# Performance work log

Hardware: AMD Instinct MI355X
Metric: run time of the kernel (lower is better)

Reference implementation:

```python
import jax, jax.numpy as jnp
import numpy as np
import math

IN_DIM = 3
N_LEVELS = 16
N_FEATS = 2
LOG2_HASHMAP = 19
BASE_RES = 16
DESIRED_RES = 2048
N_POINTS = 1048576
# first in_dim hash primes from the torch module; all fit in uint32
PRIMES = np.array([1, 2654435761, 805459861], dtype=np.uint32)


def _level_params():
    # faithful to the torch code: growth exponent divides by (base_resolution - 1)
    beta = math.exp((math.log(DESIRED_RES) - math.log(BASE_RES)) / (BASE_RES - 1))
    res = [math.floor(BASE_RES * beta ** i) for i in range(N_LEVELS)]
    hms = [min(r ** IN_DIM, 2 ** LOG2_HASHMAP) for r in res]
    return res, hms


def setup_inputs() -> dict:
    key = jax.random.key(0)
    kx, kt = jax.random.split(key)
    x = jax.random.uniform(kx, (N_POINTS, IN_DIM), dtype=jnp.float32)
    # kaiming_uniform(a=sqrt(5)) on [hashmap, n_feats] -> bound = sqrt(1/2)
    bound = math.sqrt(0.5)
    tables = jax.random.uniform(kt, (N_LEVELS, 2 ** LOG2_HASHMAP, N_FEATS),
                                dtype=jnp.float32, minval=-bound, maxval=bound)
    return {"x": x, "tables": tables}


def _forward(x, tables):
    res, hms = _level_params()
    neighbors = np.arange(1 << IN_DIM, dtype=np.int64).reshape(-1, 1)   # [8,1]
    dims = np.arange(IN_DIM, dtype=np.int64).reshape(1, -1)             # [1,3]
    bin_mask = jnp.asarray((neighbors & (1 << dims)) == 0)              # [8,3] bool
    primes = jnp.asarray(PRIMES)                                        # [3] uint32
    outs = [x]  # include_input=True
    for l in range(N_LEVELS):
        xs = x * jnp.float32(res[l])                    # [N,3]
        xi = jnp.floor(xs).astype(jnp.int32)            # torch .long() trunc; x>=0 so floor==trunc
        xf = xs - xi.astype(xs.dtype)                   # fractional part (no grad via xi)
        xi = xi[..., None, :]                           # [N,1,3]
        xf = xf[..., None, :]                           # [N,1,3]
        idx = jnp.where(bin_mask, xi, xi + 1).astype(jnp.uint32)         # [N,8,3]
        w = jnp.prod(jnp.where(bin_mask, 1.0 - xf, xf), axis=-1, keepdims=True)  # [N,8,1]
        # hash: (idx * prime) mod 2^32 (uint32 wraparound == int64 mul & 0xFFFFFFFF), xor-fold, mod size
        h = idx * primes                                # [N,8,3] uint32
        h = h[..., 0] ^ h[..., 1] ^ h[..., 2]           # [N,8]
        h = (h % jnp.uint32(hms[l])).astype(jnp.int32)
        emb = tables[l][h]                              # [N,8,F] gather
        outs.append(jnp.sum(emb * w, axis=-2))          # [N,F]
    return jnp.concatenate(outs, axis=-1)               # [N, 3 + 16*2]


def reference(x, tables):
    return _forward(x, tables)
```

## Files before the change

kernel.cpp:

```cpp
#include <hip/hip_runtime.h>
#include <math.h>
#include <stdint.h>

#define NPTS   1048576
#define NLEV   16
#define TPB    256
#define PPT    8
#define CHUNK  (TPB * PPT)
#define ROW    35
#define TBL_ENTRIES (1u << 19)

typedef float f4 __attribute__((ext_vector_type(4)));
typedef float f2 __attribute__((ext_vector_type(2)));

struct LevelParams {
    float    resf;
    uint32_t hm;
    uint32_t is_pow2;
    uint32_t use_nt;
    uint64_t magic;
};
struct LPAll { LevelParams lv[NLEV]; };

__device__ __forceinline__ void hash_gather_point(
    float xv0, float xv1, float xv2,
    const LevelParams& P, const f2* __restrict__ tbl,
    float& acc0, float& acc1)
{
    const float xs0 = xv0 * P.resf, xs1 = xv1 * P.resf, xs2 = xv2 * P.resf;
    const float f0 = floorf(xs0), f1 = floorf(xs1), f2v = floorf(xs2);
    const float t0 = xs0 - f0, t1 = xs1 - f1, t2 = xs2 - f2v;

    const unsigned a0 = (unsigned)(int)f0;
    const unsigned a1 = a0 + 1u;
    const unsigned b0 = (unsigned)(int)f1 * 2654435761u;
    const unsigned b1 = ((unsigned)(int)f1 + 1u) * 2654435761u;
    const unsigned c0 = (unsigned)(int)f2v * 805459861u;
    const unsigned c1 = ((unsigned)(int)f2v + 1u) * 805459861u;

    const float wa0 = 1.f - t0, wa1 = t0;
    const float wb0 = 1.f - t1, wb1 = t1;
    const float wc0 = 1.f - t2, wc1 = t2;

    const uint32_t hmv  = P.hm;
    const uint32_t mask = hmv - 1u;
    const uint64_t M    = P.magic;
    const bool     p2   = (P.is_pow2 != 0);
    const bool     nt   = (P.use_nt != 0);

    unsigned hi[8];
    #pragma unroll
    for (int n = 0; n < 8; ++n) {
        unsigned h = ((n & 1) ? a1 : a0)
                   ^ ((n & 2) ? b1 : b0)
                   ^ ((n & 4) ? c1 : c0);
        if (p2) {
            hi[n] = h & mask;
        } else {
            uint64_t low = M * (uint64_t)h;
            hi[n] = (uint32_t)(((__uint128_t)low * hmv) >> 64);
        }
    }
    f2 e[8];
    #pragma unroll
    for (int n = 0; n < 8; ++n)
        e[n] = nt ? __builtin_nontemporal_load(&tbl[hi[n]]) : tbl[hi[n]];

    acc0 = 0.f; acc1 = 0.f;
    #pragma unroll
    for (int n = 0; n < 8; ++n) {
        float w = (((n & 1) ? wa1 : wa0) * ((n & 2) ? wb1 : wb0))
                  * ((n & 4) ? wc1 : wc0);
        acc0 = fmaf(e[n].x, w, acc0);
        acc1 = fmaf(e[n].y, w, acc1);
    }
}

__global__ __launch_bounds__(TPB)
void hashgrid_gather(const float* __restrict__ x,
                     const float* __restrict__ tables,
                     float* __restrict__ ws,
                     LPAll lp, int base)
{
    const int tid = threadIdx.x;
    const int lvl = base + (blockIdx.x & 7);
    const int p0  = (blockIdx.x >> 3) * CHUNK;

    const LevelParams P   = lp.lv[lvl];
    const f2*         tbl = (const f2*)(tables + (size_t)lvl * TBL_ENTRIES * 2);
    const float*      xp  = x + (size_t)p0 * 3;
    f2* wrow = (f2*)ws + (size_t)lvl * NPTS + p0;

    #pragma unroll
    for (int k = 0; k < PPT; ++k) {
        const int pi = tid + k * TPB;
        const float xv0 = __builtin_nontemporal_load(&xp[pi * 3 + 0]);
        const float xv1 = __builtin_nontemporal_load(&xp[pi * 3 + 1]);
        const float xv2 = __builtin_nontemporal_load(&xp[pi * 3 + 2]);
        float acc0, acc1;
        hash_gather_point(xv0, xv1, xv2, P, tbl, acc0, acc1);
        f2 v; v.x = acc0; v.y = acc1;
        __builtin_nontemporal_store(v, &wrow[pi]);
    }
}

__global__ __launch_bounds__(TPB)
void hashgrid_interleave(const float* __restrict__ x,
                         const float* __restrict__ ws,
                         float* __restrict__ out)
{
    __shared__ float srow[TPB * ROW];
    const int tid = threadIdx.x;
    const int p0  = blockIdx.x * TPB;

    const float* xblk = x + (size_t)p0 * 3;
    #pragma unroll
    for (int j = 0; j < 3; ++j) {
        int idx = tid + j * TPB;
        int p = idx / 3, c = idx - p * 3;
        srow[p * ROW + c] = __builtin_nontemporal_load(&xblk[idx]);
    }
    const f2* wsv = (const f2*)ws;
    #pragma unroll
    for (int l = 0; l < NLEV; ++l) {
        f2 v = __builtin_nontemporal_load(&wsv[(size_t)l * NPTS + p0 + tid]);
        srow[tid * ROW + 3 + 2 * l] = v.x;
        srow[tid * ROW + 4 + 2 * l] = v.y;
    }
    __syncthreads();

    f4*       outv = (f4*)(out + (size_t)p0 * ROW);
    const f4* sv   = (const f4*)srow;
    for (int j = tid; j < (TPB * ROW) / 4; j += TPB)
        __builtin_nontemporal_store(sv[j], &outv[j]);
}

__global__ __launch_bounds__(TPB)
void hashgrid_lvl(const float* __restrict__ x,
                  const float* __restrict__ tables,
                  float* __restrict__ out,
                  LPAll lp, int base)
{
    const int tid = threadIdx.x;
    const int lvl = base + (blockIdx.x & 7);
    const int p0  = (blockIdx.x >> 3) * TPB;

    const float* xp = x + (size_t)p0 * 3;
    const float xv0 = xp[tid * 3 + 0];
    const float xv1 = xp[tid * 3 + 1];
    const float xv2 = xp[tid * 3 + 2];

    const LevelParams P   = lp.lv[lvl];
    const f2*         tbl = (const f2*)(tables + (size_t)lvl * TBL_ENTRIES * 2);
    float acc0, acc1;
    hash_gather_point(xv0, xv1, xv2, P, tbl, acc0, acc1);

    float* orow = out + (size_t)(p0 + tid) * ROW;
    __builtin_nontemporal_store(acc0, &orow[3 + 2 * lvl]);
    __builtin_nontemporal_store(acc1, &orow[4 + 2 * lvl]);
    if (lvl == 0) {
        __builtin_nontemporal_store(xv0, &orow[0]);
        __builtin_nontemporal_store(xv1, &orow[1]);
        __builtin_nontemporal_store(xv2, &orow[2]);
    }
}

extern "C" void kernel_launch(void* const* d_in, const int* in_sizes, int n_in,
                              void* d_out, int out_size, void* d_ws, size_t ws_size,
                              hipStream_t stream)
{
    const float* x      = (const float*)d_in[0];
    const float* tables = (const float*)d_in[1];
    float*       out    = (float*)d_out;

    LPAll lp;
    const double beta = exp((log(2048.0) - log(16.0)) / 15.0);
    for (int i = 0; i < NLEV; ++i) {
        double r = floor(16.0 * pow(beta, (double)i));
        double h3 = r * r * r;
        uint32_t hm = (h3 < (double)(1u << 19)) ? (uint32_t)h3 : (1u << 19);
        lp.lv[i].resf    = (float)r;
        lp.lv[i].hm      = hm;
        lp.lv[i].is_pow2 = ((hm & (hm - 1u)) == 0u) ? 1u : 0u;
        lp.lv[i].use_nt  = ((size_t)hm * 8 > (1u << 20)) ? 1u : 0u;
        lp.lv[i].magic   = lp.lv[i].is_pow2 ? 0ull : (~0ull / hm + 1ull);
    }

    const size_t ws_need = (size_t)NLEV * NPTS * 2 * sizeof(float);
    if (ws_size >= ws_need) {
        const int gblocks = 8 * (NPTS / CHUNK);
        hashgrid_gather<<<gblocks, TPB, 0, stream>>>(x, tables, (float*)d_ws, lp, 0);
        hashgrid_gather<<<gblocks, TPB, 0, stream>>>(x, tables, (float*)d_ws, lp, 8);
        hashgrid_interleave<<<NPTS / TPB, TPB, 0, stream>>>(x, (const float*)d_ws, out);
    } else {
        const int nblocks = 8 * (NPTS / TPB);
        hashgrid_lvl<<<nblocks, TPB, 0, stream>>>(x, tables, out, lp, 0);
        hashgrid_lvl<<<nblocks, TPB, 0, stream>>>(x, tables, out, lp, 8);
    }
}
```

Measured before the change: 494.1 us.

## Fetch x-neighbour pairs with one 16-byte load on power-of-two levels

For levels whose table size is a power of two, the hash of the x+1 corner differs from the x corner only in bit 0 when the integer x coordinate is even. The code loads an aligned float4 covering both entries and selects components by parity, issuing the second set of gathers only for odd coordinates. This is meant to cut the number of random table gathers by about a quarter. In exchange it adds divergence on the parity branch and wider loads.

```diff
diff --git a/kernel.cpp b/kernel.cpp
--- a/kernel.cpp
+++ b/kernel.cpp
@@ -22,7 +22,7 @@
 };
 struct LPAll { LevelParams lv[NLEV]; };
 
-__device__ __forceinline__ void hash_gather_point(
+__device__ __forceinline__ void hash_gather_generic(
     float xv0, float xv1, float xv2,
     const LevelParams& P, const f2* __restrict__ tbl,
     float& acc0, float& acc1)
@@ -42,11 +42,9 @@
     const float wb0 = 1.f - t1, wb1 = t1;
     const float wc0 = 1.f - t2, wc1 = t2;
 
-    const uint32_t hmv  = P.hm;
-    const uint32_t mask = hmv - 1u;
-    const uint64_t M    = P.magic;
-    const bool     p2   = (P.is_pow2 != 0);
-    const bool     nt   = (P.use_nt != 0);
+    const uint32_t hmv = P.hm;
+    const uint64_t M   = P.magic;
+    const bool     nt  = (P.use_nt != 0);
 
     unsigned hi[8];
     #pragma unroll
@@ -54,12 +52,8 @@
         unsigned h = ((n & 1) ? a1 : a0)
                    ^ ((n & 2) ? b1 : b0)
                    ^ ((n & 4) ? c1 : c0);
-        if (p2) {
-            hi[n] = h & mask;
-        } else {
-            uint64_t low = M * (uint64_t)h;
-            hi[n] = (uint32_t)(((__uint128_t)low * hmv) >> 64);
-        }
+        uint64_t low = M * (uint64_t)h;
+        hi[n] = (uint32_t)(((__uint128_t)low * hmv) >> 64);
     }
     f2 e[8];
     #pragma unroll
@@ -76,6 +70,77 @@
     }
 }
 
+__device__ __forceinline__ void hash_gather_pow2(
+    float xv0, float xv1, float xv2,
+    const LevelParams& P, const f4* __restrict__ tbl4,
+    float& acc0, float& acc1)
+{
+    const float xs0 = xv0 * P.resf, xs1 = xv1 * P.resf, xs2 = xv2 * P.resf;
+    const float f0 = floorf(xs0), f1 = floorf(xs1), f2v = floorf(xs2);
+    const float t0 = xs0 - f0, t1 = xs1 - f1, t2 = xs2 - f2v;
+
+    const unsigned a0 = (unsigned)(int)f0;
+    const unsigned a1 = a0 + 1u;
+    const unsigned b0 = (unsigned)(int)f1 * 2654435761u;
+    const unsigned b1 = ((unsigned)(int)f1 + 1u) * 2654435761u;
+    const unsigned c0 = (unsigned)(int)f2v * 805459861u;
+    const unsigned c1 = ((unsigned)(int)f2v + 1u) * 805459861u;
+
+    const float wa0 = 1.f - t0, wa1 = t0;
+    const float wb0 = 1.f - t1, wb1 = t1;
+    const float wc0 = 1.f - t2, wc1 = t2;
+
+    const uint32_t mask = P.hm - 1u;
+    const bool     nt   = (P.use_nt != 0);
+
+    unsigned s[4]; float wp[4];
+    s[0] = b0 ^ c0;  wp[0] = wb0 * wc0;
+    s[1] = b1 ^ c0;  wp[1] = wb1 * wc0;
+    s[2] = b0 ^ c1;  wp[2] = wb0 * wc1;
+    s[3] = b1 ^ c1;  wp[3] = wb1 * wc1;
+
+    unsigned hl[4], hh[4];
+    #pragma unroll
+    for (int j = 0; j < 4; ++j) {
+        hl[j] = (a0 ^ s[j]) & mask;
+        hh[j] = (a1 ^ s[j]) & mask;
+    }
+
+    f4 q[4];
+    #pragma unroll
+    for (int j = 0; j < 4; ++j)
+        q[j] = nt ? __builtin_nontemporal_load(&tbl4[hl[j] >> 1])
+                  : tbl4[hl[j] >> 1];
+
+    f4 qh[4];
+    #pragma unroll
+    for (int j = 0; j < 4; ++j) qh[j] = q[j];
+
+    if (a0 & 1u) {
+        #pragma unroll
+        for (int j = 0; j < 4; ++j)
+            qh[j] = nt ? __builtin_nontemporal_load(&tbl4[hh[j] >> 1])
+                       : tbl4[hh[j] >> 1];
+    }
+
+    acc0 = 0.f; acc1 = 0.f;
+    #pragma unroll
+    for (int j = 0; j < 4; ++j) {
+        const bool sl = (hl[j] & 1u);
+        const bool sh = (hh[j] & 1u);
+        const float elo0 = sl ? q[j].z  : q[j].x;
+        const float elo1 = sl ? q[j].w  : q[j].y;
+        const float ehi0 = sh ? qh[j].z : qh[j].x;
+        const float ehi1 = sh ? qh[j].w : qh[j].y;
+        const float wl = wa0 * wp[j];
+        const float wh = wa1 * wp[j];
+        acc0 = fmaf(elo0, wl, acc0);
+        acc1 = fmaf(elo1, wl, acc1);
+        acc0 = fmaf(ehi0, wh, acc0);
+        acc1 = fmaf(ehi1, wh, acc1);
+    }
+}
+
 __global__ __launch_bounds__(TPB)
 void hashgrid_gather(const float* __restrict__ x,
                      const float* __restrict__ tables,
@@ -87,20 +152,36 @@
     const int p0  = (blockIdx.x >> 3) * CHUNK;
 
     const LevelParams P   = lp.lv[lvl];
-    const f2*         tbl = (const f2*)(tables + (size_t)lvl * TBL_ENTRIES * 2);
+    const float*      tb  = tables + (size_t)lvl * TBL_ENTRIES * 2;
     const float*      xp  = x + (size_t)p0 * 3;
     f2* wrow = (f2*)ws + (size_t)lvl * NPTS + p0;
 
-    #pragma unroll
-    for (int k = 0; k < PPT; ++k) {
-        const int pi = tid + k * TPB;
-        const float xv0 = __builtin_nontemporal_load(&xp[pi * 3 + 0]);
-        const float xv1 = __builtin_nontemporal_load(&xp[pi * 3 + 1]);
-        const float xv2 = __builtin_nontemporal_load(&xp[pi * 3 + 2]);
-        float acc0, acc1;
-        hash_gather_point(xv0, xv1, xv2, P, tbl, acc0, acc1);
-        f2 v; v.x = acc0; v.y = acc1;
-        __builtin_nontemporal_store(v, &wrow[pi]);
+    if (P.is_pow2) {
+        const f4* tbl4 = (const f4*)tb;
+        #pragma unroll
+        for (int k = 0; k < PPT; ++k) {
+            const int pi = tid + k * TPB;
+            const float xv0 = __builtin_nontemporal_load(&xp[pi * 3 + 0]);
+            const float xv1 = __builtin_nontemporal_load(&xp[pi * 3 + 1]);
+            const float xv2 = __builtin_nontemporal_load(&xp[pi * 3 + 2]);
+            float acc0, acc1;
+            hash_gather_pow2(xv0, xv1, xv2, P, tbl4, acc0, acc1);
+            f2 v; v.x = acc0; v.y = acc1;
+            __builtin_nontemporal_store(v, &wrow[pi]);
+        }
+    } else {
+        const f2* tbl = (const f2*)tb;
+        #pragma unroll
+        for (int k = 0; k < PPT; ++k) {
+            const int pi = tid + k * TPB;
+            const float xv0 = __builtin_nontemporal_load(&xp[pi * 3 + 0]);
+            const float xv1 = __builtin_nontemporal_load(&xp[pi * 3 + 1]);
+            const float xv2 = __builtin_nontemporal_load(&xp[pi * 3 + 2]);
+            float acc0, acc1;
+            hash_gather_generic(xv0, xv1, xv2, P, tbl, acc0, acc1);
+            f2 v; v.x = acc0; v.y = acc1;
+            __builtin_nontemporal_store(v, &wrow[pi]);
+        }
     }
 }
 
@@ -150,10 +231,11 @@
     const float xv1 = xp[tid * 3 + 1];
     const float xv2 = xp[tid * 3 + 2];
 
-    const LevelParams P   = lp.lv[lvl];
-    const f2*         tbl = (const f2*)(tables + (size_t)lvl * TBL_ENTRIES * 2);
+    const LevelParams P  = lp.lv[lvl];
+    const float*      tb = tables + (size_t)lvl * TBL_ENTRIES * 2;
     float acc0, acc1;
-    hash_gather_point(xv0, xv1, xv2, P, tbl, acc0, acc1);
+    if (P.is_pow2) hash_gather_pow2(xv0, xv1, xv2, P, (const f4*)tb, acc0, acc1);
+    else           hash_gather_generic(xv0, xv1, xv2, P, (const f2*)tb, acc0, acc1);
 
     float* orow = out + (size_t)(p0 + tid) * ROW;
     __builtin_nontemporal_store(acc0, &orow[3 + 2 * lvl]);
```

After: 549.1 us. 1.11x slower.
